# Optimization experiments

Measured on AMD Instinct MI355X. Metric: run time of the kernel, lower is better.

The kernel has to match this reference:

```python
import jax, jax.numpy as jnp
import numpy as np


def setup_inputs() -> dict:
    key = jax.random.key(0)
    k1, k2, k3, k4 = jax.random.split(key, 4)
    N, F_in, F_out = 8192, 512, 256
    inp = jax.random.normal(k1, (N, F_in), dtype=jnp.float32)
    adj = jax.random.uniform(k2, (N, N), dtype=jnp.float32)
    stdv = 1.0 / np.sqrt(F_out)
    weight = jax.random.uniform(k3, (F_in, F_out), minval=-stdv, maxval=stdv, dtype=jnp.float32)
    b = jax.random.uniform(k4, (F_out,), minval=-stdv, maxval=stdv, dtype=jnp.float32)
    return {"input": inp, "adj": adj, "weight": weight, "b": b}


def reference(input, adj, weight, b):
    N = adj.shape[0]
    degree = jnp.sum(adj, axis=1)                      # [N]
    # A_tilde = 2*I - adj
    A_tilde = 2.0 * jnp.eye(N, dtype=adj.dtype) - adj
    d_inv_sqrt = 1.0 / jnp.sqrt(2.0 + degree)          # [N]
    # D^-1/2 @ A_tilde @ D^-1/2 as broadcasted row/col scaling (same math, O(N^2))
    L_sharpen = d_inv_sqrt[:, None] * A_tilde * d_inv_sqrt[None, :]
    support = input @ weight                           # [N, F_out]
    out = L_sharpen @ support + b                      # [N, F_out]
    return jax.nn.relu(out)
```

## Files before the change

kernel.cpp:

```cpp
#include <hip/hip_runtime.h>


typedef _Float16 h4 __attribute__((ext_vector_type(4)));
typedef _Float16 h8 __attribute__((ext_vector_type(8)));
typedef float f4 __attribute__((ext_vector_type(4)));

__device__ __forceinline__ void gload_lds16(const void* g, void* l) {
    __builtin_amdgcn_global_load_lds(
        (const __attribute__((address_space(1))) void*)g,
        (__attribute__((address_space(3))) void*)l, 16, 0, 0);
}
__device__ __forceinline__ void gload2(const float* p, f4& x, f4& y) {
    asm volatile("global_load_dwordx4 %0, %2, off\n\t"
                 "global_load_dwordx4 %1, %2, off offset:16"
                 : "=&v"(x), "=&v"(y) : "v"(p) : "memory");
}
__device__ __forceinline__ void gloadBfrag(const char* p, h8& x, h8& y) {
    asm volatile("global_load_dwordx4 %0, %2, off\n\t"
                 "global_load_dwordx4 %1, %2, off offset:1024"
                 : "=&v"(x), "=&v"(y) : "v"(p) : "memory");
}

__global__ __launch_bounds__(256) void k0_wt(const float* __restrict__ weight,
                                             char* __restrict__ wt) {
    const int idx = blockIdx.x * 256 + threadIdx.x;
    const int k = idx >> 8, j = idx & 255;
    const _Float16 h = (_Float16)weight[idx];
    const int off = j * 1024 + ((k >> 6) << 7) + (((k & 63) << 1) ^ ((j & 7) << 4));
    *(_Float16*)(wt + off) = h;
}

__global__ __launch_bounds__(256) void k1_deg(const float* __restrict__ adj,
                                              float* __restrict__ dinv) {
    const int r = blockIdx.x;
    const float4* rp = (const float4*)(adj + (size_t)r * 8192);
    const int t = threadIdx.x;
    float s = 0.f;
#pragma unroll
    for (int i = 0; i < 8; ++i) {
        float4 v = rp[t + i * 256];
        s += (v.x + v.y) + (v.z + v.w);
    }
#pragma unroll
    for (int off = 32; off > 0; off >>= 1) s += __shfl_down(s, off, 64);
    __shared__ float part[4];
    if ((t & 63) == 0) part[t >> 6] = s;
    __syncthreads();
    if (t == 0) {
        float deg = (part[0] + part[1]) + (part[2] + part[3]);
        dinv[r] = 1.0f / sqrtf(2.0f + deg);
    }
}

__global__ __launch_bounds__(512) void k2_support(const float* __restrict__ input,
                                                  const char* __restrict__ wt,
                                                  const float* __restrict__ dinv,
                                                  char* __restrict__ sT) {
    __shared__ char smem[4096 + 32768];
    const int t = threadIdx.x, w = t >> 6, l = t & 63;
    const int r0 = (int)blockIdx.x * 32;
    const int arow = t >> 4, ak4 = t & 15;
    const int bj = l >> 3, bb = (l & 7) * 16;

    f4 acc[2][2] = {};

    for (int kt = 0; kt < 8; ++kt) {
        const int k0 = kt * 64;
        __syncthreads();
        {
            float4 v = *(const float4*)(input + (size_t)(r0 + arow) * 512 + k0 + ak4 * 4);
            h4 h;
            h[0] = (_Float16)v.x; h[1] = (_Float16)v.y;
            h[2] = (_Float16)v.z; h[3] = (_Float16)v.w;
            *(h4*)(smem + arow * 128 + ((ak4 * 8) ^ ((arow & 7) << 4))) = h;
        }
#pragma unroll
        for (int q = 0; q < 4; ++q) {
            const int c = q * 8 + w;
            gload_lds16(wt + (size_t)(c * 8 + bj) * 1024 + kt * 128 + bb,
                        smem + 4096 + c * 1024);
        }
        __syncthreads();
#pragma unroll
        for (int kk = 0; kk < 2; ++kk) {
            const int ko = kk * 64 + ((l >> 4) << 4);
            h8 a[2], b[2];
#pragma unroll
            for (int m = 0; m < 2; ++m) {
                const int r = m * 16 + (l & 15);
                a[m] = *(const h8*)(smem + r * 128 + (ko ^ ((r & 7) << 4)));
            }
#pragma unroll
            for (int n = 0; n < 2; ++n) {
                const int j = w * 32 + n * 16 + (l & 15);
                b[n] = *(const h8*)(smem + 4096 + j * 128 + (ko ^ ((j & 7) << 4)));
            }
#pragma unroll
            for (int m = 0; m < 2; ++m)
#pragma unroll
                for (int n = 0; n < 2; ++n)
                    acc[m][n] = __builtin_amdgcn_mfma_f32_16x16x32_f16(a[m], b[n], acc[m][n], 0, 0, 0);
        }
    }
#pragma unroll
    for (int m = 0; m < 2; ++m)
#pragma unroll
        for (int n = 0; n < 2; ++n) {
            const int j = w * 32 + n * 16 + (l & 15);
            const int k0r = r0 + m * 16 + ((l >> 4) << 2);
            h4 h;
#pragma unroll
            for (int r = 0; r < 4; ++r)
                h[r] = (_Float16)(dinv[k0r + r] * acc[m][n][r]);
            const int off = (((j >> 4) * 128 + (k0r >> 6)) << 11) +
                            (((k0r >> 5) & 1) << 10) +
                            ((((k0r >> 3) & 3) << 4) + (j & 15)) * 16 +
                            ((k0r & 7) << 1);
            *(h4*)(sT + off) = h;
        }
}

__global__ __launch_bounds__(512, 4) void k3_spmm(const float* __restrict__ adj,
                                                  const char* __restrict__ sT,
                                                  float* __restrict__ part,
                                                  float* __restrict__ out,
                                                  int steps) {
    __shared__ __align__(16) char smem[2][8192];
    const int t = threadIdx.x;
    const int w = t >> 6, l = t & 63;
    const int i0 = (127 - (int)blockIdx.x) * 64;
    const int ks0 = (int)blockIdx.y * steps * 64;
    const int dkt = (i0 - ks0) >> 6;

    const int arow = t >> 3;
    const int ak8 = (t & 7) * 8;
    const int arow_g = i0 + arow;
    const float* aptr = adj + (size_t)arow_g * 8192 + ks0 + ak8;
    const int a_off = arow * 128 + (((t & 7) << 4) ^ ((arow & 7) << 4));

    const char* bpn0 = sT + ((size_t)(w * 2) * 128 + (ks0 >> 6)) * 2048 + l * 16;
    const char* bpn1 = bpn0 + 262144;

    f4 acc[4][2] = {};
    h8 bvA[2][2], bvB[2][2];
    f4 ax0, ay0, ax1, ay1;

    auto loadB = [&](int kt, h8 (&bv)[2][2]) {
        gloadBfrag(bpn0 + (size_t)kt * 2048, bv[0][0], bv[1][0]);
        gloadBfrag(bpn1 + (size_t)kt * 2048, bv[0][1], bv[1][1]);
    };
    auto writeA = [&](char* buf, int kt, const f4 x, const f4 y) {
        const int kg = ks0 + kt * 64 + ak8;
        h8 h;
        if (kt == dkt) {
#pragma unroll
            for (int e = 0; e < 4; ++e)
                h[e] = (_Float16)((arow_g == kg + e) ? 2.0f - x[e] : -x[e]);
#pragma unroll
            for (int e = 0; e < 4; ++e)
                h[4 + e] = (_Float16)((arow_g == kg + 4 + e) ? 2.0f - y[e] : -y[e]);
        } else {
#pragma unroll
            for (int e = 0; e < 4; ++e) h[e] = (_Float16)(-x[e]);
#pragma unroll
            for (int e = 0; e < 4; ++e) h[4 + e] = (_Float16)(-y[e]);
        }
        *(h8*)(buf + a_off) = h;
    };
    auto compute = [&](const char* A, const h8 (&bv)[2][2]) {
#pragma unroll
        for (int kk = 0; kk < 2; ++kk) {
            const int ko = kk * 64 + ((l >> 4) << 4);
            h8 a[4];
#pragma unroll
            for (int m = 0; m < 4; ++m) {
                const int r = m * 16 + (l & 15);
                a[m] = *(const h8*)(A + r * 128 + (ko ^ ((r & 7) << 4)));
            }
#pragma unroll
            for (int m = 0; m < 4; ++m)
#pragma unroll
                for (int n = 0; n < 2; ++n)
                    acc[m][n] = __builtin_amdgcn_mfma_f32_16x16x32_f16(a[m], bv[kk][n], acc[m][n], 0, 0, 0);
        }
    };

#define SBAR0() __builtin_amdgcn_sched_barrier(0)
#define WAIT_ADJ(N, X, Y)                                                     \
    asm volatile("s_waitcnt vmcnt(" #N ")" : "+v"(X), "+v"(Y) :: "memory");   \
    SBAR0();
#define WAIT_STEP(N, X, Y, BV)                                                \
    asm volatile("s_waitcnt vmcnt(" #N ")"                                    \
                 : "+v"(X), "+v"(Y), "+v"(BV[0][0]), "+v"(BV[0][1]),          \
                   "+v"(BV[1][0]), "+v"(BV[1][1]) :: "memory");               \
    SBAR0();
#define WAIT_BV(N, BV)                                                        \
    asm volatile("s_waitcnt vmcnt(" #N ")"                                    \
                 : "+v"(BV[0][0]), "+v"(BV[0][1]),                            \
                   "+v"(BV[1][0]), "+v"(BV[1][1]) :: "memory");               \
    SBAR0();
#define BARRIER()                                                             \
    asm volatile("s_waitcnt lgkmcnt(0)\n\ts_barrier" ::: "memory");           \
    SBAR0();

    gload2(aptr, ax0, ay0);
    loadB(0, bvA);
    WAIT_ADJ(4, ax0, ay0)
    writeA(smem[0], 0, ax0, ay0);
    gload2(aptr + 64, ax1, ay1);
    BARRIER()

#define BODY(kt, XC, YC, XN, YN, BVC, BVN, BUFC, BUFN)                        \
    {                                                                         \
        loadB((kt) + 1, BVN);                                                 \
        gload2(aptr + (size_t)((kt) + 2) * 64, XC, YC);                       \
        WAIT_STEP(6, XN, YN, BVC)                                             \
        writeA(BUFN, (kt) + 1, XN, YN);                                       \
        compute(BUFC, BVC);                                                   \
        BARRIER()                                                             \
    }

    for (int kt2 = 0; kt2 + 2 <= steps - 2; kt2 += 2) {
        BODY(kt2,     ax0, ay0, ax1, ay1, bvA, bvB, smem[0], smem[1])
        BODY(kt2 + 1, ax1, ay1, ax0, ay0, bvB, bvA, smem[1], smem[0])
    }
    {
        loadB(steps - 1, bvB);
        WAIT_STEP(4, ax1, ay1, bvA)
        writeA(smem[1], steps - 1, ax1, ay1);
        compute(smem[0], bvA);
        BARRIER()
    }
    {
        WAIT_BV(0, bvB)
        compute(smem[1], bvB);
    }
#undef BODY
#undef WAIT_ADJ
#undef WAIT_STEP
#undef WAIT_BV
#undef BARRIER
#undef SBAR0

    float* dst = (blockIdx.y == gridDim.y - 1) ? out
               : part + (size_t)blockIdx.y * (8192 * 256);
#pragma unroll
    for (int m = 0; m < 4; ++m)
#pragma unroll
        for (int n = 0; n < 2; ++n) {
            const int j = w * 32 + n * 16 + (l & 15);
            const int ib = i0 + m * 16 + ((l >> 4) << 2);
#pragma unroll
            for (int r = 0; r < 4; ++r)
                dst[(size_t)(ib + r) * 256 + j] = acc[m][n][r];
        }
}

__global__ __launch_bounds__(256) void k4_fin(const float* __restrict__ part,
                                              float* __restrict__ out,
                                              const float* __restrict__ dinv,
                                              const float* __restrict__ bias,
                                              int nsplit) {
    const int idx = blockIdx.x * 256 + threadIdx.x;
    float4 s = ((const float4*)out)[idx];
    for (int sp = 0; sp < nsplit - 1; ++sp)
        s += ((const float4*)(part + (size_t)sp * (8192 * 256)))[idx];
    const float dv = dinv[idx >> 6];
    const float4 b = ((const float4*)bias)[idx & 63];
    float4 r;
    r.x = fmaxf(dv * s.x + b.x, 0.f);
    r.y = fmaxf(dv * s.y + b.y, 0.f);
    r.z = fmaxf(dv * s.z + b.z, 0.f);
    r.w = fmaxf(dv * s.w + b.w, 0.f);
    ((float4*)out)[idx] = r;
}

extern "C" void kernel_launch(void* const* d_in, const int* in_sizes, int n_in,
                              void* d_out, int out_size, void* d_ws, size_t ws_size,
                              hipStream_t stream) {
    const float* input  = (const float*)d_in[0];
    const float* adj    = (const float*)d_in[1];
    const float* weight = (const float*)d_in[2];
    const float* bias   = (const float*)d_in[3];
    float* out = (float*)d_out;

    char* ws = (char*)d_ws;
    float* dinv = (float*)ws;
    char*  wt   = ws + 32768;
    char*  sT   = ws + 294912;
    float* part = (float*)(ws + 294912 + 4194304);

    const size_t base = 294912 + 4194304;
    int nsplit = 1;
    if (ws_size >= base + 7ull * 8388608) nsplit = 8;
    else if (ws_size >= base + 3 * 8388608) nsplit = 4;
    else if (ws_size >= base + 1 * 8388608) nsplit = 2;
    const int steps = 128 / nsplit;

    k0_wt<<<512, 256, 0, stream>>>(weight, wt);
    k1_deg<<<8192, 256, 0, stream>>>(adj, dinv);
    k2_support<<<256, 512, 0, stream>>>(input, wt, dinv, sT);
    k3_spmm<<<dim3(128, nsplit), 512, 0, stream>>>(adj, sT, part, out, steps);
    k4_fin<<<2048, 256, 0, stream>>>(part, out, dinv, bias, nsplit);
}
```

Before: 149.6 us.

## Store split-K partials in fp16, cap split at 4, add MFMA priority

Split-K partial sums are now written and read as fp16 instead of fp32, which halves the traffic for the partial buffers between the SpMM and finalize kernels. The maximum split drops from 8 to 4. The compute section raises wave priority around the MFMA block, and the block-to-row mapping is no longer reversed. The fp16 partials lose some accuracy, and fewer splits mean fewer workgroups in flight to hide the latency of streaming adj.

```diff
diff --git a/kernel.cpp b/kernel.cpp
--- a/kernel.cpp
+++ b/kernel.cpp
@@ -122,13 +122,13 @@
 
 __global__ __launch_bounds__(512, 4) void k3_spmm(const float* __restrict__ adj,
                                                   const char* __restrict__ sT,
-                                                  float* __restrict__ part,
+                                                  _Float16* __restrict__ parth,
                                                   float* __restrict__ out,
                                                   int steps) {
     __shared__ __align__(16) char smem[2][8192];
     const int t = threadIdx.x;
     const int w = t >> 6, l = t & 63;
-    const int i0 = (127 - (int)blockIdx.x) * 64;
+    const int i0 = (int)blockIdx.x * 64;
     const int ks0 = (int)blockIdx.y * steps * 64;
     const int dkt = (i0 - ks0) >> 6;
 
@@ -168,6 +168,7 @@
         *(h8*)(buf + a_off) = h;
     };
     auto compute = [&](const char* A, const h8 (&bv)[2][2]) {
+        __builtin_amdgcn_s_setprio(1);
 #pragma unroll
         for (int kk = 0; kk < 2; ++kk) {
             const int ko = kk * 64 + ((l >> 4) << 4);
@@ -183,6 +184,7 @@
                 for (int n = 0; n < 2; ++n)
                     acc[m][n] = __builtin_amdgcn_mfma_f32_16x16x32_f16(a[m], bv[kk][n], acc[m][n], 0, 0, 0);
         }
+        __builtin_amdgcn_s_setprio(0);
     };
 
 #define SBAR0() __builtin_amdgcn_sched_barrier(0)
@@ -242,29 +244,44 @@
 #undef BARRIER
 #undef SBAR0
 
-    float* dst = (blockIdx.y == gridDim.y - 1) ? out
-               : part + (size_t)blockIdx.y * (8192 * 256);
-#pragma unroll
-    for (int m = 0; m < 4; ++m)
-#pragma unroll
-        for (int n = 0; n < 2; ++n) {
-            const int j = w * 32 + n * 16 + (l & 15);
-            const int ib = i0 + m * 16 + ((l >> 4) << 2);
-#pragma unroll
-            for (int r = 0; r < 4; ++r)
-                dst[(size_t)(ib + r) * 256 + j] = acc[m][n][r];
-        }
-}
-
-__global__ __launch_bounds__(256) void k4_fin(const float* __restrict__ part,
+    if (blockIdx.y == gridDim.y - 1) {
+#pragma unroll
+        for (int m = 0; m < 4; ++m)
+#pragma unroll
+            for (int n = 0; n < 2; ++n) {
+                const int j = w * 32 + n * 16 + (l & 15);
+                const int ib = i0 + m * 16 + ((l >> 4) << 2);
+#pragma unroll
+                for (int r = 0; r < 4; ++r)
+                    out[(size_t)(ib + r) * 256 + j] = acc[m][n][r];
+            }
+    } else {
+        _Float16* pslot = parth + (size_t)blockIdx.y * (8192 * 256);
+#pragma unroll
+        for (int m = 0; m < 4; ++m)
+#pragma unroll
+            for (int n = 0; n < 2; ++n) {
+                const int j = w * 32 + n * 16 + (l & 15);
+                const int ib = i0 + m * 16 + ((l >> 4) << 2);
+#pragma unroll
+                for (int r = 0; r < 4; ++r)
+                    pslot[(size_t)(ib + r) * 256 + j] = (_Float16)acc[m][n][r];
+            }
+    }
+}
+
+__global__ __launch_bounds__(256) void k4_fin(const _Float16* __restrict__ parth,
                                               float* __restrict__ out,
                                               const float* __restrict__ dinv,
                                               const float* __restrict__ bias,
                                               int nsplit) {
     const int idx = blockIdx.x * 256 + threadIdx.x;
     float4 s = ((const float4*)out)[idx];
-    for (int sp = 0; sp < nsplit - 1; ++sp)
-        s += ((const float4*)(part + (size_t)sp * (8192 * 256)))[idx];
+    for (int sp = 0; sp < nsplit - 1; ++sp) {
+        const h4 p = *(const h4*)(parth + (size_t)sp * (8192 * 256) + (size_t)idx * 4);
+        s.x += (float)p[0]; s.y += (float)p[1];
+        s.z += (float)p[2]; s.w += (float)p[3];
+    }
     const float dv = dinv[idx >> 6];
     const float4 b = ((const float4*)bias)[idx & 63];
     float4 r;
@@ -285,21 +302,20 @@
     float* out = (float*)d_out;
 
     char* ws = (char*)d_ws;
-    float* dinv = (float*)ws;
-    char*  wt   = ws + 32768;
-    char*  sT   = ws + 294912;
-    float* part = (float*)(ws + 294912 + 4194304);
+    float*    dinv  = (float*)ws;
+    char*     wt    = ws + 32768;
+    char*     sT    = ws + 294912;
+    _Float16* parth = (_Float16*)(ws + 294912 + 4194304);
 
     const size_t base = 294912 + 4194304;
     int nsplit = 1;
-    if (ws_size >= base + 7ull * 8388608) nsplit = 8;
-    else if (ws_size >= base + 3 * 8388608) nsplit = 4;
-    else if (ws_size >= base + 1 * 8388608) nsplit = 2;
+    if (ws_size >= base + 3ull * 4194304) nsplit = 4;
+    else if (ws_size >= base + 1ull * 4194304) nsplit = 2;
     const int steps = 128 / nsplit;
 
     k0_wt<<<512, 256, 0, stream>>>(weight, wt);
     k1_deg<<<8192, 256, 0, stream>>>(adj, dinv);
     k2_support<<<256, 512, 0, stream>>>(input, wt, dinv, sT);
-    k3_spmm<<<dim3(128, nsplit), 512, 0, stream>>>(adj, sT, part, out, steps);
-    k4_fin<<<2048, 256, 0, stream>>>(part, out, dinv, bias, nsplit);
-}
+    k3_spmm<<<dim3(128, nsplit), 512, 0, stream>>>(adj, sT, parth, out, steps);
+    k4_fin<<<2048, 256, 0, stream>>>(parth, out, dinv, bias, nsplit);
+}
```

Result: faster. 127.7 us (-14.6%).
